# Optimization experiments

Measured on AMD Instinct MI355X. Metric: run time of the kernel, lower is better.

The kernel has to match this reference:

```python
import jax, jax.numpy as jnp
import numpy as np

TEMPERATURE = 0.07
PRED_STEPS = (1, 2)


def setup_inputs() -> dict:
    key = jax.random.key(0)
    ks = jax.random.split(key, 6)
    N, L, Ct, Cp = 128, 1024, 512, 512
    scale = 0.05
    return {
        "timesteps": jax.random.normal(ks[0], (N, L, Ct), jnp.float32) * scale,
        "patient_timesteps": jax.random.normal(ks[1], (N, L, Cp), jnp.float32) * scale,
        "W1": jax.random.normal(ks[2], (Ct, Cp), jnp.float32) * scale,
        "b1": jax.random.normal(ks[3], (Ct,), jnp.float32) * scale,
        "W2": jax.random.normal(ks[4], (Ct, Cp), jnp.float32) * scale,
        "b2": jax.random.normal(ks[5], (Ct,), jnp.float32) * scale,
    }


def _step_logits(timesteps, patient_timesteps, W, b, step):
    # _patient_timesteps: [N, L-step, Cp]; _timesteps: [N, L-step, Ct]
    p = patient_timesteps[:, :-step]
    t = timesteps[:, step:]
    pred = jnp.einsum('nlp,cp->nlc', p, W) + b  # linear predictor
    # all-pairs similarity per timestep: [N(query), M(candidate), L]
    l_neg = jnp.einsum('nlc,mlc->nml', t, pred)
    return l_neg


def _nce_acc(l_neg):
    # vectorized replacement of the per-sample python loop with .cpu() syncs
    n = jax.lax.stop_gradient(l_neg)
    N = n.shape[0]
    idx = jnp.arange(N)
    pos = n[idx, idx]  # [N, L]
    eye = jnp.eye(N, dtype=bool)[:, :, None]
    greater = jnp.where(eye, True, pos[:, None, :] > n)  # [N, M, L]
    return jnp.mean(jnp.all(greater, axis=1).astype(jnp.float32))


def reference(timesteps, patient_timesteps, W1, b1, W2, b2):
    params = [(W1, b1), (W2, b2)]
    logits, accs = [], []
    for step, (W, b) in zip(PRED_STEPS, params):
        l_neg = _step_logits(timesteps, patient_timesteps, W, b, step)
        accs.append(_nce_acc(l_neg))
        logits.append(l_neg / TEMPERATURE)
    accs = jnp.stack(accs)
    logits = jnp.concatenate(logits, axis=-1)  # [N, N, sum_s(L-s)]
    N = logits.shape[0]
    y_trues = jnp.broadcast_to(jnp.arange(N)[:, None], (N, logits.shape[-1]))
    return logits, y_trues, accs
```

## Files before the change

kernel.cpp:

```cpp
#include <hip/hip_runtime.h>
#include <stdint.h>

typedef short bf16x8 __attribute__((ext_vector_type(8)));
typedef float f32x4 __attribute__((ext_vector_type(4)));

#define LOGITS_SZ 33505280u
#define YT_SZ     261760u
#define ACC_OFF   33767040u
#define PRED_ELEMS 67108864ull
#define TEMP_INV  (1.0f/0.07f)

#define WBF_OFF   0ull
#define PRED_OFF  524288ull
#define CTMP_OFF  (PRED_OFF + 2*PRED_ELEMS)
#define PBF_OFF   (CTMP_OFF + 33554432ull)
#define TBF_OFF   (PBF_OFF + 67108864ull)
#define BIG_USH   (TBF_OFF + 67108864ull)

__device__ inline ushort f2bf(float f) {
  uint32_t u = __float_as_uint(f);
  u = (u + 0x7fffu + ((u >> 16) & 1u)) >> 16;
  return (ushort)u;
}
__device__ inline float bf2f(ushort h) { return __uint_as_float(((uint32_t)h) << 16); }
__device__ inline uint32_t pack2(float a, float b) {
  return (uint32_t)f2bf(a) | ((uint32_t)f2bf(b) << 16);
}
__device__ inline void gl_lds16(const ushort* g, ushort* l) {
  __builtin_amdgcn_global_load_lds(
      (const __attribute__((address_space(1))) uint32_t*)g,
      (__attribute__((address_space(3))) uint32_t*)l, 16, 0, 0);
}

__global__ void init_misc(float* __restrict__ out) {
  uint32_t i = blockIdx.x * 256u + threadIdx.x;
  if (i < YT_SZ) out[LOGITS_SZ + i] = (float)(i / 2045u);
  if (i < 2u) out[ACC_OFF + i] = 0.0f;
}

__global__ void cast_w(const float* __restrict__ w1, const float* __restrict__ w2,
                       ushort* __restrict__ wbf) {
  uint32_t i = blockIdx.x * 256u + threadIdx.x;
  float v = (i < 262144u) ? w1[i] : w2[i - 262144u];
  wbf[i] = f2bf(v);
}

__global__ void cast_all(const float* __restrict__ p, const float* __restrict__ t,
                         const float* __restrict__ w1, const float* __restrict__ w2,
                         ushort* __restrict__ pbf, ushort* __restrict__ tbf,
                         ushort* __restrict__ wbf) {
  size_t c = (size_t)blockIdx.x * 256u + threadIdx.x;
  const float* src; ushort* dst; size_t off;
  if (c < 8388608ull)            { src = p;  dst = pbf; off = c * 8; }
  else if (c < 16777216ull)      { src = t;  dst = tbf; off = (c - 8388608ull) * 8; }
  else {
    size_t cc = c - 16777216ull;
    if (cc < 32768ull) { src = w1; dst = wbf;          off = cc * 8; }
    else               { src = w2; dst = wbf + 262144; off = (cc - 32768ull) * 8; }
  }
  float4 f0 = *(const float4*)(src + off), f1 = *(const float4*)(src + off + 4);
  uint4 v = make_uint4(pack2(f0.x, f0.y), pack2(f0.z, f0.w),
                       pack2(f1.x, f1.y), pack2(f1.z, f1.w));
  *(uint4*)(dst + off) = v;
}

template<bool PRED, bool ABF>
__global__ __launch_bounds__(256, 3)
void gemm_kernel(const float* __restrict__ af32, const ushort* __restrict__ abf,
                 const ushort* __restrict__ bmat, const float* __restrict__ b1,
                 const float* __restrict__ b2, ushort* __restrict__ outp)
{
  __shared__ __align__(16) ushort As[128 * 32];
  __shared__ __align__(16) ushort Bs[128 * 32];
  __shared__ __align__(16) ushort Sb[128 * 128];

  const int t = threadIdx.x;
  const int lane = t & 63, w = t >> 6;
  const int q = lane >> 4, c16 = lane & 15;
  const int wr = (w & 1) * 64, wc = (w >> 1) * 64;

  size_t a_off, a_stride, ostride;
  const ushort* bbase; ushort* obase;
  const float* bias = nullptr;

  if (PRED) {
    int id = blockIdx.x;
    int x = id & 7, p = id >> 3;
    int y = x + 8 * (p >> 3);
    int sct = p & 7, s = sct >> 2, ct = sct & 3;
    int r0 = y * 128, m = y >> 3, l0 = (y & 7) * 128;
    a_off = (size_t)r0 * 512; a_stride = 512;
    bbase = bmat + (size_t)s * 262144 + (size_t)ct * 128 * 512;
    obase = outp + (size_t)s * PRED_ELEMS + ((size_t)l0 * 128 + m) * 512 + ct * 128;
    ostride = 65536;
    bias = (s ? b2 : b1) + ct * 128;
  } else {
    int id = blockIdx.x;
    int x = id & 7, p = id >> 3;
    int g = x + 8 * (p >> 1), s01 = p & 1;
    int l = g - s01;
    if (l < 0 || l > (s01 ? 1021 : 1022)) return;
    int lc = g + 1;
    a_off = (size_t)lc * 512; a_stride = 524288;
    bbase = bmat + (size_t)s01 * PRED_ELEMS + (size_t)l * 65536;
    obase = outp + ((size_t)s01 * 1024 + l) * 16384;
    ostride = 128;
  }

  f32x4 acc[4][4] = {};

  const int ar = t >> 1, ah = t & 1;
  const float* asrcf = ABF ? nullptr : (af32 + a_off + (size_t)ar * a_stride + ah * 16);
  const int fr = (ar >> 1) & 3;
  const int drow = lane >> 2;
  const int dcol = (lane & 3) * 8;

  for (int kk = 0; kk < 16; ++kk) {
    const int p0 = kk * 32;
    if (ABF) {
      const ushort* ab = abf + a_off + p0 + dcol;
      gl_lds16(ab + (size_t)(w * 16 + drow) * a_stride,      &As[w * 512]);
      gl_lds16(ab + (size_t)(64 + w * 16 + drow) * a_stride, &As[2048 + w * 512]);
    } else {
      const float4* af = (const float4*)(asrcf + p0);
      float4 f0 = af[0], f1 = af[1], f2 = af[2], f3 = af[3];
      uint4 v0 = make_uint4(pack2(f0.x, f0.y), pack2(f0.z, f0.w), pack2(f1.x, f1.y), pack2(f1.z, f1.w));
      uint4 v1 = make_uint4(pack2(f2.x, f2.y), pack2(f2.z, f2.w), pack2(f3.x, f3.y), pack2(f3.z, f3.w));
      *(uint4*)&As[ar * 32 + (((2 * ah)     ^ fr) << 3)] = v0;
      *(uint4*)&As[ar * 32 + (((2 * ah + 1) ^ fr) << 3)] = v1;
    }
    {
      const ushort* bb = bbase + p0 + dcol;
      gl_lds16(bb + (size_t)(w * 16 + drow) * 512,      &Bs[w * 512]);
      gl_lds16(bb + (size_t)(64 + w * 16 + drow) * 512, &Bs[2048 + w * 512]);
    }
    __syncthreads();
    bf16x8 a[4], b[4];
#pragma unroll
    for (int i = 0; i < 4; ++i) {
      int row = wr + i * 16 + c16;
      a[i] = ABF ? *(const bf16x8*)&As[row * 32 + q * 8]
                 : *(const bf16x8*)&As[row * 32 + ((q ^ ((row >> 1) & 3)) << 3)];
      int col = wc + i * 16 + c16;
      b[i] = *(const bf16x8*)&Bs[col * 32 + q * 8];
    }
#pragma unroll
    for (int i = 0; i < 4; ++i)
#pragma unroll
      for (int j = 0; j < 4; ++j)
        acc[i][j] = __builtin_amdgcn_mfma_f32_16x16x32_bf16(a[i], b[j], acc[i][j], 0, 0, 0);
    __syncthreads();
  }

#pragma unroll
  for (int j = 0; j < 4; ++j) {
    int col = wc + j * 16 + c16;
    float bj = PRED ? bias[col] : 0.0f;
#pragma unroll
    for (int i = 0; i < 4; ++i)
#pragma unroll
      for (int rr = 0; rr < 4; ++rr) {
        int row = wr + i * 16 + q * 4 + rr;
        Sb[row * 128 + col] = f2bf(acc[i][j][rr] + bj);
      }
  }
  __syncthreads();
#pragma unroll
  for (int it = 0; it < 8; ++it) {
    int idx = it * 256 + t;
    int row = idx >> 4, c8 = (idx & 15) * 8;
    *(uint4*)(obase + (size_t)row * ostride + c8) = *(const uint4*)&Sb[row * 128 + c8];
  }
}

__global__ void transpose_kernel(const ushort* __restrict__ ctmp, float* __restrict__ out)
{
  const int nmt = blockIdx.x, lt = blockIdx.y, s01 = blockIdx.z;
  const int Ls = s01 ? 1022 : 1023;
  const int lbase = s01 ? 1023 : 0;
  const int t = threadIdx.x;
  __shared__ float T[64][65];
  {
    int i = t >> 2, j0 = (t & 3) * 16;
    const ushort* src = ctmp + ((size_t)(s01 * 1024 + lt * 64 + i)) * 16384 + nmt * 64 + j0;
    uint4 v0 = *(const uint4*)src;
    uint4 v1 = *(const uint4*)(src + 8);
    float* dst = &T[i][j0];
    uint32_t wsv[8] = {v0.x, v0.y, v0.z, v0.w, v1.x, v1.y, v1.z, v1.w};
#pragma unroll
    for (int e = 0; e < 8; ++e) {
      dst[2 * e]     = bf2f((ushort)(wsv[e] & 0xffffu));
      dst[2 * e + 1] = bf2f((ushort)(wsv[e] >> 16));
    }
  }
  __syncthreads();
  {
    int nm = t >> 2, l0 = (t & 3) * 16;
    size_t obase = (size_t)(nmt * 64 + nm) * 2045 + lbase + lt * 64 + l0;
#pragma unroll
    for (int k = 0; k < 16; ++k) {
      int lg = lt * 64 + l0 + k;
      if (lg < Ls) out[obase + k] = T[l0 + k][nm] * TEMP_INV;
    }
  }
}

__global__ void acc_kernel(const ushort* __restrict__ ctmp, float* __restrict__ accbuf)
{
  const int idx = blockIdx.x;
  const int s01 = idx & 1;
  const int l = idx >> 1;
  const int t = threadIdx.x;
  const ushort* base = ctmp + ((size_t)s01 * 1024 + (size_t)l) * 16384;
  const int n = t >> 1, half = t & 1;
  const ushort* row = base + n * 128 + half * 64;
  float mx = -1e30f;
#pragma unroll
  for (int k8 = 0; k8 < 8; ++k8) {
    uint4 v = *(const uint4*)(row + k8 * 8);
    uint32_t wsv[4] = {v.x, v.y, v.z, v.w};
#pragma unroll
    for (int e = 0; e < 4; ++e) {
      int m0 = half * 64 + k8 * 8 + e * 2;
      float a0 = bf2f((ushort)(wsv[e] & 0xffffu));
      float a1 = bf2f((ushort)(wsv[e] >> 16));
      if (m0 != n)     mx = fmaxf(mx, a0);
      if (m0 + 1 != n) mx = fmaxf(mx, a1);
    }
  }
  float pos = bf2f(base[n * 128 + n]);
  mx = fmaxf(mx, __shfl_xor(mx, 1, 64));
  int ok = (half == 0 && pos > mx) ? 1 : 0;
  for (int off = 32; off > 0; off >>= 1) ok += __shfl_down(ok, off, 64);
  __shared__ int partial[4];
  if ((t & 63) == 0) partial[t >> 6] = ok;
  __syncthreads();
  if (t == 0) {
    int sum = partial[0] + partial[1] + partial[2] + partial[3];
    atomicAdd(&accbuf[s01], (float)sum);
  }
}

__global__ void scale_kernel(float* accbuf) {
  if (threadIdx.x == 0) accbuf[0] *= (1.0f / 130944.0f);
  if (threadIdx.x == 1) accbuf[1] *= (1.0f / 130816.0f);
}

extern "C" void kernel_launch(void* const* d_in, const int* in_sizes, int n_in,
                              void* d_out, int out_size, void* d_ws, size_t ws_size,
                              hipStream_t stream)
{
  const float* tsteps  = (const float*)d_in[0];
  const float* patient = (const float*)d_in[1];
  const float* W1 = (const float*)d_in[2];
  const float* b1 = (const float*)d_in[3];
  const float* W2 = (const float*)d_in[4];
  const float* b2 = (const float*)d_in[5];
  float* out = (float*)d_out;
  ushort* wsp  = (ushort*)d_ws;
  ushort* wbf  = wsp + WBF_OFF;
  ushort* pred = wsp + PRED_OFF;
  ushort* ctmp = wsp + CTMP_OFF;

  const bool big = ws_size >= BIG_USH * 2ull;

  init_misc<<<1023, 256, 0, stream>>>(out);
  if (big) {
    ushort* pbf = wsp + PBF_OFF;
    ushort* tbf = wsp + TBF_OFF;
    cast_all<<<65792, 256, 0, stream>>>(patient, tsteps, W1, W2, pbf, tbf, wbf);
    gemm_kernel<true, true><<<8192, 256, 0, stream>>>(nullptr, pbf, wbf, b1, b2, pred);
    gemm_kernel<false, true><<<2048, 256, 0, stream>>>(nullptr, tbf, pred, nullptr, nullptr, ctmp);
  } else {
    cast_w<<<2048, 256, 0, stream>>>(W1, W2, wbf);
    gemm_kernel<true, false><<<8192, 256, 0, stream>>>(patient, nullptr, wbf, b1, b2, pred);
    gemm_kernel<false, false><<<2048, 256, 0, stream>>>(tsteps, nullptr, pred, nullptr, nullptr, ctmp);
  }
  transpose_kernel<<<dim3(256, 16, 2), 256, 0, stream>>>(ctmp, out);
  acc_kernel<<<2045, 256, 0, stream>>>(ctmp, out + ACC_OFF);
  scale_kernel<<<1, 64, 0, stream>>>(out + ACC_OFF);
}
```

Measured before the change: 1.083 ms.

## Fuse predictor GEMM into per-timestep similarity GEMM, keeping pred in LDS

Replaces the two-GEMM pipeline, which wrote a full bf16 pred tensor to global memory and read it back, with one fused kernel. Each block computes the 128x128 pred tile for one timestep, chunk by chunk, into a swizzled LDS buffer and immediately consumes it for the all-pairs similarity. The cast kernel now writes p and t in an [L, N, C] layout so a block's rows are contiguous, and the transpose store is reorganised for coalesced writes along L. The small-workspace fallback is removed, and occupancy drops to 2 blocks per SM because of the larger accumulator and register state.

```diff
diff --git a/kernel.cpp b/kernel.cpp
--- a/kernel.cpp
+++ b/kernel.cpp
@@ -7,15 +7,12 @@
 #define LOGITS_SZ 33505280u
 #define YT_SZ     261760u
 #define ACC_OFF   33767040u
-#define PRED_ELEMS 67108864ull
 #define TEMP_INV  (1.0f/0.07f)
 
 #define WBF_OFF   0ull
-#define PRED_OFF  524288ull
-#define CTMP_OFF  (PRED_OFF + 2*PRED_ELEMS)
+#define CTMP_OFF  524288ull
 #define PBF_OFF   (CTMP_OFF + 33554432ull)
 #define TBF_OFF   (PBF_OFF + 67108864ull)
-#define BIG_USH   (TBF_OFF + 67108864ull)
 
 __device__ inline ushort f2bf(float f) {
   uint32_t u = __float_as_uint(f);
@@ -36,13 +33,6 @@
   uint32_t i = blockIdx.x * 256u + threadIdx.x;
   if (i < YT_SZ) out[LOGITS_SZ + i] = (float)(i / 2045u);
   if (i < 2u) out[ACC_OFF + i] = 0.0f;
-}
-
-__global__ void cast_w(const float* __restrict__ w1, const float* __restrict__ w2,
-                       ushort* __restrict__ wbf) {
-  uint32_t i = blockIdx.x * 256u + threadIdx.x;
-  float v = (i < 262144u) ? w1[i] : w2[i - 262144u];
-  wbf[i] = f2bf(v);
 }
 
 __global__ void cast_all(const float* __restrict__ p, const float* __restrict__ t,
@@ -50,118 +40,132 @@
                          ushort* __restrict__ pbf, ushort* __restrict__ tbf,
                          ushort* __restrict__ wbf) {
   size_t c = (size_t)blockIdx.x * 256u + threadIdx.x;
-  const float* src; ushort* dst; size_t off;
-  if (c < 8388608ull)            { src = p;  dst = pbf; off = c * 8; }
-  else if (c < 16777216ull)      { src = t;  dst = tbf; off = (c - 8388608ull) * 8; }
-  else {
+  const float* src; ushort* dst; size_t soff, doff;
+  if (c < 16777216ull) {
+    size_t cc = c;
+    if (cc < 8388608ull) { src = p; dst = pbf; }
+    else                 { src = t; dst = tbf; cc -= 8388608ull; }
+    size_t pb = cc & 63, l = (cc >> 6) & 1023, m = cc >> 16;
+    soff = cc * 8;
+    doff = ((l << 7) + m) * 512 + pb * 8;
+  } else {
     size_t cc = c - 16777216ull;
-    if (cc < 32768ull) { src = w1; dst = wbf;          off = cc * 8; }
-    else               { src = w2; dst = wbf + 262144; off = (cc - 32768ull) * 8; }
-  }
-  float4 f0 = *(const float4*)(src + off), f1 = *(const float4*)(src + off + 4);
+    if (cc < 32768ull) { src = w1; dst = wbf; }
+    else               { src = w2; dst = wbf + 262144; cc -= 32768ull; }
+    soff = cc * 8; doff = soff;
+  }
+  float4 f0 = *(const float4*)(src + soff), f1 = *(const float4*)(src + soff + 4);
   uint4 v = make_uint4(pack2(f0.x, f0.y), pack2(f0.z, f0.w),
                        pack2(f1.x, f1.y), pack2(f1.z, f1.w));
-  *(uint4*)(dst + off) = v;
-}
-
-template<bool PRED, bool ABF>
-__global__ __launch_bounds__(256, 3)
-void gemm_kernel(const float* __restrict__ af32, const ushort* __restrict__ abf,
-                 const ushort* __restrict__ bmat, const float* __restrict__ b1,
-                 const float* __restrict__ b2, ushort* __restrict__ outp)
+  *(uint4*)(dst + doff) = v;
+}
+
+__global__ __launch_bounds__(256, 2)
+void fused_kernel(const ushort* __restrict__ pbf, const ushort* __restrict__ tbf,
+                  const ushort* __restrict__ wbf, const float* __restrict__ b1,
+                  const float* __restrict__ b2, ushort* __restrict__ ctmp)
 {
   __shared__ __align__(16) ushort As[128 * 32];
   __shared__ __align__(16) ushort Bs[128 * 32];
-  __shared__ __align__(16) ushort Sb[128 * 128];
+  __shared__ __align__(16) ushort Ps[128 * 128];
 
   const int t = threadIdx.x;
   const int lane = t & 63, w = t >> 6;
   const int q = lane >> 4, c16 = lane & 15;
   const int wr = (w & 1) * 64, wc = (w >> 1) * 64;
 
-  size_t a_off, a_stride, ostride;
-  const ushort* bbase; ushort* obase;
-  const float* bias = nullptr;
-
-  if (PRED) {
-    int id = blockIdx.x;
-    int x = id & 7, p = id >> 3;
-    int y = x + 8 * (p >> 3);
-    int sct = p & 7, s = sct >> 2, ct = sct & 3;
-    int r0 = y * 128, m = y >> 3, l0 = (y & 7) * 128;
-    a_off = (size_t)r0 * 512; a_stride = 512;
-    bbase = bmat + (size_t)s * 262144 + (size_t)ct * 128 * 512;
-    obase = outp + (size_t)s * PRED_ELEMS + ((size_t)l0 * 128 + m) * 512 + ct * 128;
-    ostride = 65536;
-    bias = (s ? b2 : b1) + ct * 128;
-  } else {
-    int id = blockIdx.x;
-    int x = id & 7, p = id >> 3;
-    int g = x + 8 * (p >> 1), s01 = p & 1;
-    int l = g - s01;
-    if (l < 0 || l > (s01 ? 1021 : 1022)) return;
-    int lc = g + 1;
-    a_off = (size_t)lc * 512; a_stride = 524288;
-    bbase = bmat + (size_t)s01 * PRED_ELEMS + (size_t)l * 65536;
-    obase = outp + ((size_t)s01 * 1024 + l) * 16384;
-    ostride = 128;
-  }
-
-  f32x4 acc[4][4] = {};
-
-  const int ar = t >> 1, ah = t & 1;
-  const float* asrcf = ABF ? nullptr : (af32 + a_off + (size_t)ar * a_stride + ah * 16);
-  const int fr = (ar >> 1) & 3;
+  int id = blockIdx.x;
+  int x = id & 7, pp = id >> 3;
+  int g = x + 8 * (pp >> 1), s01 = pp & 1;
+  int l = g - s01;
+  if (l < 0 || l > (s01 ? 1021 : 1022)) return;
+  int lc = g + 1;
+
+  const ushort* abase = pbf + (size_t)l * 65536;
+  const ushort* tbase = tbf + (size_t)lc * 65536;
+  const ushort* wbase = wbf + (size_t)s01 * 262144;
+  const float* bias = s01 ? b2 : b1;
+  ushort* obase = ctmp + ((size_t)s01 * 1024 + (size_t)l) * 16384;
+
   const int drow = lane >> 2;
   const int dcol = (lane & 3) * 8;
 
-  for (int kk = 0; kk < 16; ++kk) {
-    const int p0 = kk * 32;
-    if (ABF) {
-      const ushort* ab = abf + a_off + p0 + dcol;
-      gl_lds16(ab + (size_t)(w * 16 + drow) * a_stride,      &As[w * 512]);
-      gl_lds16(ab + (size_t)(64 + w * 16 + drow) * a_stride, &As[2048 + w * 512]);
-    } else {
-      const float4* af = (const float4*)(asrcf + p0);
-      float4 f0 = af[0], f1 = af[1], f2 = af[2], f3 = af[3];
-      uint4 v0 = make_uint4(pack2(f0.x, f0.y), pack2(f0.z, f0.w), pack2(f1.x, f1.y), pack2(f1.z, f1.w));
-      uint4 v1 = make_uint4(pack2(f2.x, f2.y), pack2(f2.z, f2.w), pack2(f3.x, f3.y), pack2(f3.z, f3.w));
-      *(uint4*)&As[ar * 32 + (((2 * ah)     ^ fr) << 3)] = v0;
-      *(uint4*)&As[ar * 32 + (((2 * ah + 1) ^ fr) << 3)] = v1;
-    }
-    {
-      const ushort* bb = bbase + p0 + dcol;
-      gl_lds16(bb + (size_t)(w * 16 + drow) * 512,      &Bs[w * 512]);
-      gl_lds16(bb + (size_t)(64 + w * 16 + drow) * 512, &Bs[2048 + w * 512]);
-    }
+  f32x4 acc2[4][4] = {};
+
+  for (int ct = 0; ct < 4; ++ct) {
+    f32x4 acc1[4][4] = {};
+    const ushort* wct = wbase + (size_t)ct * 65536;
+    for (int kk = 0; kk < 16; ++kk) {
+      const int p0 = kk * 32;
+      { const ushort* ab = abase + p0 + dcol;
+        gl_lds16(ab + (size_t)(w * 16 + drow) * 512,      &As[w * 512]);
+        gl_lds16(ab + (size_t)(64 + w * 16 + drow) * 512, &As[2048 + w * 512]); }
+      { const ushort* bb = wct + p0 + dcol;
+        gl_lds16(bb + (size_t)(w * 16 + drow) * 512,      &Bs[w * 512]);
+        gl_lds16(bb + (size_t)(64 + w * 16 + drow) * 512, &Bs[2048 + w * 512]); }
+      __syncthreads();
+      bf16x8 a[4], b[4];
+#pragma unroll
+      for (int i = 0; i < 4; ++i) {
+        a[i] = *(const bf16x8*)&As[(wr + i * 16 + c16) * 32 + q * 8];
+        b[i] = *(const bf16x8*)&Bs[(wc + i * 16 + c16) * 32 + q * 8];
+      }
+#pragma unroll
+      for (int i = 0; i < 4; ++i)
+#pragma unroll
+        for (int j = 0; j < 4; ++j)
+          acc1[i][j] = __builtin_amdgcn_mfma_f32_16x16x32_bf16(a[i], b[j], acc1[i][j], 0, 0, 0);
+      __syncthreads();
+    }
+#pragma unroll
+    for (int j = 0; j < 4; ++j) {
+      int col = wc + j * 16 + c16;
+      float bj = bias[ct * 128 + col];
+#pragma unroll
+      for (int i = 0; i < 4; ++i)
+#pragma unroll
+        for (int rr = 0; rr < 4; ++rr) {
+          int row = wr + i * 16 + q * 4 + rr;
+          Ps[row * 128 + (col ^ ((row & 7) << 3))] = f2bf(acc1[i][j][rr] + bj);
+        }
+    }
+    { const ushort* ab = tbase + ct * 128 + dcol;
+      gl_lds16(ab + (size_t)(w * 16 + drow) * 512,      &As[w * 512]);
+      gl_lds16(ab + (size_t)(64 + w * 16 + drow) * 512, &As[2048 + w * 512]); }
     __syncthreads();
-    bf16x8 a[4], b[4];
-#pragma unroll
-    for (int i = 0; i < 4; ++i) {
-      int row = wr + i * 16 + c16;
-      a[i] = ABF ? *(const bf16x8*)&As[row * 32 + q * 8]
-                 : *(const bf16x8*)&As[row * 32 + ((q ^ ((row >> 1) & 3)) << 3)];
-      int col = wc + i * 16 + c16;
-      b[i] = *(const bf16x8*)&Bs[col * 32 + q * 8];
-    }
-#pragma unroll
-    for (int i = 0; i < 4; ++i)
-#pragma unroll
-      for (int j = 0; j < 4; ++j)
-        acc[i][j] = __builtin_amdgcn_mfma_f32_16x16x32_bf16(a[i], b[j], acc[i][j], 0, 0, 0);
-    __syncthreads();
+#pragma unroll
+    for (int kk2 = 0; kk2 < 4; ++kk2) {
+      bf16x8 a[4], b[4];
+#pragma unroll
+      for (int i = 0; i < 4; ++i) {
+        a[i] = *(const bf16x8*)&As[(wr + i * 16 + c16) * 32 + q * 8];
+        int col = wc + i * 16 + c16;
+        b[i] = *(const bf16x8*)&Ps[col * 128 + ((kk2 * 32 + q * 8) ^ ((col & 7) << 3))];
+      }
+#pragma unroll
+      for (int i = 0; i < 4; ++i)
+#pragma unroll
+        for (int j = 0; j < 4; ++j)
+          acc2[i][j] = __builtin_amdgcn_mfma_f32_16x16x32_bf16(a[i], b[j], acc2[i][j], 0, 0, 0);
+      __syncthreads();
+      if (kk2 < 3) {
+        const ushort* ab = tbase + ct * 128 + (kk2 + 1) * 32 + dcol;
+        gl_lds16(ab + (size_t)(w * 16 + drow) * 512,      &As[w * 512]);
+        gl_lds16(ab + (size_t)(64 + w * 16 + drow) * 512, &As[2048 + w * 512]);
+        __syncthreads();
+      }
+    }
   }
 
 #pragma unroll
   for (int j = 0; j < 4; ++j) {
     int col = wc + j * 16 + c16;
-    float bj = PRED ? bias[col] : 0.0f;
 #pragma unroll
     for (int i = 0; i < 4; ++i)
 #pragma unroll
       for (int rr = 0; rr < 4; ++rr) {
         int row = wr + i * 16 + q * 4 + rr;
-        Sb[row * 128 + col] = f2bf(acc[i][j][rr] + bj);
+        Ps[row * 128 + col] = f2bf(acc2[i][j][rr]);
       }
   }
   __syncthreads();
@@ -169,7 +173,7 @@
   for (int it = 0; it < 8; ++it) {
     int idx = it * 256 + t;
     int row = idx >> 4, c8 = (idx & 15) * 8;
-    *(uint4*)(obase + (size_t)row * ostride + c8) = *(const uint4*)&Sb[row * 128 + c8];
+    *(uint4*)(obase + (size_t)row * 128 + c8) = *(const uint4*)&Ps[row * 128 + c8];
   }
 }
 
@@ -195,12 +199,15 @@
   }
   __syncthreads();
   {
-    int nm = t >> 2, l0 = (t & 3) * 16;
-    size_t obase = (size_t)(nmt * 64 + nm) * 2045 + lbase + lt * 64 + l0;
-#pragma unroll
-    for (int k = 0; k < 16; ++k) {
-      int lg = lt * 64 + l0 + k;
-      if (lg < Ls) out[obase + k] = T[l0 + k][nm] * TEMP_INV;
+    int ll = t & 63, nm0 = t >> 6;
+    int lg = lt * 64 + ll;
+    if (lg < Ls) {
+      size_t ob = (size_t)lbase + lg;
+#pragma unroll
+      for (int pass = 0; pass < 16; ++pass) {
+        int nm = pass * 4 + nm0;
+        out[(size_t)(nmt * 64 + nm) * 2045 + ob] = T[ll][nm] * TEMP_INV;
+      }
     }
   }
 }
@@ -259,23 +266,13 @@
   float* out = (float*)d_out;
   ushort* wsp  = (ushort*)d_ws;
   ushort* wbf  = wsp + WBF_OFF;
-  ushort* pred = wsp + PRED_OFF;
   ushort* ctmp = wsp + CTMP_OFF;
-
-  const bool big = ws_size >= BIG_USH * 2ull;
+  ushort* pbf  = wsp + PBF_OFF;
+  ushort* tbf  = wsp + TBF_OFF;
 
   init_misc<<<1023, 256, 0, stream>>>(out);
-  if (big) {
-    ushort* pbf = wsp + PBF_OFF;
-    ushort* tbf = wsp + TBF_OFF;
-    cast_all<<<65792, 256, 0, stream>>>(patient, tsteps, W1, W2, pbf, tbf, wbf);
-    gemm_kernel<true, true><<<8192, 256, 0, stream>>>(nullptr, pbf, wbf, b1, b2, pred);
-    gemm_kernel<false, true><<<2048, 256, 0, stream>>>(nullptr, tbf, pred, nullptr, nullptr, ctmp);
-  } else {
-    cast_w<<<2048, 256, 0, stream>>>(W1, W2, wbf);
-    gemm_kernel<true, false><<<8192, 256, 0, stream>>>(patient, nullptr, wbf, b1, b2, pred);
-    gemm_kernel<false, false><<<2048, 256, 0, stream>>>(tsteps, nullptr, pred, nullptr, nullptr, ctmp);
-  }
+  cast_all<<<65792, 256, 0, stream>>>(patient, tsteps, W1, W2, pbf, tbf, wbf);
+  fused_kernel<<<2048, 256, 0, stream>>>(pbf, tbf, wbf, b1, b2, ctmp);
   transpose_kernel<<<dim3(256, 16, 2), 256, 0, stream>>>(ctmp, out);
   acc_kernel<<<2045, 256, 0, stream>>>(ctmp, out + ACC_OFF);
   scale_kernel<<<1, 64, 0, stream>>>(out + ACC_OFF);
```

New measurement: 917.0 us. -15.3%, faster.
